# Kernel tuning notes

Measured on AMD Instinct MI355X. Metric: run time of the kernel, lower is better.

## Reference

```python
import jax, jax.numpy as jnp
import numpy as np

IB = 8      # input/hidden activation bits
ABMVM = 8   # gate activation bits after MVM
ABNM = 8    # near-memory compute bits
NL = 0.05   # analog noise level
CY_DIV = 2.0
CY_SCALE = 2.0


def quant_pass(x, wb, sign):
    # Faithful port of QuantFunc.forward: clip/clamp then fake-quant (round to grid).
    if wb is None or wb == 0:
        return x
    if sign:
        delta = 0.0 if wb == 1 else 1.0 / (2.0 ** (wb - 1))
        x = jnp.clip(x, -1.0 + delta, 1.0 - delta)
    else:
        x = jnp.clip(x, 0.0, 1.0)
    if wb == 1:
        return jnp.sign(x)
    scale = 2.0 ** (wb - 1) if sign else 2.0 ** wb
    return jnp.round(x * scale) / scale


def setup_inputs() -> dict:
    key = jax.random.key(0)
    ks = jax.random.split(key, 7)
    B, I, H = 4096, 1024, 1024
    return {
        "input": jax.random.normal(ks[0], (B, I), jnp.float32),
        "hx": jax.random.normal(ks[1], (B, H), jnp.float32),
        "cx": jax.random.normal(ks[2], (B, H), jnp.float32),
        "weight_ih": jax.random.normal(ks[3], (4 * H, I), jnp.float32) * 0.1,
        "weight_hh": jax.random.normal(ks[4], (4 * H, H), jnp.float32) * 0.1,
        "bias_ih": jax.random.normal(ks[5], (4 * H,), jnp.float32) * 0.1,
        "bias_hh": jax.random.normal(ks[6], (4 * H,), jnp.float32) * 0.1,
        "train": 0,
    }


def reference(input, hx, cx, weight_ih, weight_hh, bias_ih, bias_hh, train):
    # Per-call Gaussian noise (simulated analog hardware); fixed key for reproducibility.
    nk = jax.random.split(jax.random.key(42), 4)
    noise_w_ih = jax.random.normal(nk[0], weight_ih.T.shape, weight_ih.dtype) * weight_ih.max() * NL
    noise_w_hh = jax.random.normal(nk[1], weight_hh.T.shape, weight_hh.dtype) * weight_hh.max() * NL
    noise_b_ih = jax.random.normal(nk[2], bias_ih.shape, bias_ih.dtype) * bias_ih.max() * NL
    noise_b_hh = jax.random.normal(nk[3], bias_hh.shape, bias_hh.dtype) * bias_hh.max() * NL

    # gates: [B, 4H]
    gates = (quant_pass(input, IB, True) @ (weight_ih.T + noise_w_ih) + bias_ih + noise_b_ih
             + quant_pass(hx, IB, True) @ (weight_hh.T + noise_w_hh) + bias_hh + noise_b_hh)

    ingate, forgetgate, cellgate, outgate = jnp.split(gates, 4, axis=1)
    ingate = quant_pass(jax.nn.sigmoid(ingate), ABMVM, False)
    forgetgate = quant_pass(jax.nn.sigmoid(forgetgate), ABMVM, False)
    cellgate = quant_pass(jnp.tanh(cellgate), ABMVM, True)
    outgate = quant_pass(jax.nn.sigmoid(outgate), ABMVM, False)

    cy = quant_pass((quant_pass(forgetgate * cx, ABNM, True)
                     + quant_pass(ingate * cellgate, ABNM, True)) / CY_DIV, ABNM, True)
    hy = quant_pass(outgate * quant_pass(jnp.tanh(cy * CY_SCALE), ABNM, True), ABNM, True)
    return (hy, cy)
```

## Files before the change

### kernel.cpp

```cpp
#include <hip/hip_runtime.h>
#include <hip/hip_bf16.h>
#include <stdint.h>
#include <stddef.h>


#define PART 1

typedef __attribute__((ext_vector_type(8))) short bf16x8;
typedef __attribute__((ext_vector_type(4))) float f32x4;

#define BATCH 4096

#define WS_A_OFF    ((size_t)0)
#define WS_B_OFF    ((size_t)16 << 20)
#define WS_BIAS_OFF ((size_t)48 << 20)
#define WS_MAX_OFF  (WS_BIAS_OFF + 16384)

__host__ __device__ inline void tf2x32(uint32_t k0, uint32_t k1,
                                       uint32_t x0, uint32_t x1,
                                       uint32_t &o0, uint32_t &o1)
{
  const uint32_t k2 = k0 ^ k1 ^ 0x1BD11BDAu;
#define TFR(r) { x0 += x1; x1 = (x1 << (r)) | (x1 >> (32 - (r))); x1 ^= x0; }
  x0 += k0; x1 += k1;
  TFR(13) TFR(15) TFR(26) TFR(6)
  x0 += k1; x1 += k2 + 1u;
  TFR(17) TFR(29) TFR(16) TFR(24)
  x0 += k2; x1 += k0 + 2u;
  TFR(13) TFR(15) TFR(26) TFR(6)
  x0 += k0; x1 += k1 + 3u;
  TFR(17) TFR(29) TFR(16) TFR(24)
  x0 += k1; x1 += k2 + 4u;
  TFR(13) TFR(15) TFR(26) TFR(6)
  x0 += k2; x1 += k0 + 5u;
#undef TFR
  o0 = x0; o1 = x1;
}

__device__ inline uint32_t jax_bits32(uint32_t k0, uint32_t k1, uint32_t i, uint32_t size)
{
#if PART
  uint32_t a, b;
  tf2x32(k0, k1, 0u, i, a, b);
  return a ^ b;
#else
  uint32_t half = size >> 1, a, b;
  if (i < half) { tf2x32(k0, k1, i, i + half, a, b); return a; }
  tf2x32(k0, k1, i - half, i, a, b); return b;
#endif
}

__device__ inline float bits_to_normal(uint32_t bits)
{
  float f = __uint_as_float((bits >> 9) | 0x3F800000u) - 1.0f;
  const float lo = -0x1.fffffep-1f;
  float u = fmaxf(lo, f * 2.0f + lo);
  float w = -log1pf(-u * u);
  float p;
  if (w < 5.0f) {
    w -= 2.5f;
    p = 2.81022636e-08f;
    p = fmaf(p, w, 3.43273939e-07f);
    p = fmaf(p, w, -3.5233877e-06f);
    p = fmaf(p, w, -4.39150654e-06f);
    p = fmaf(p, w, 0.00021858087f);
    p = fmaf(p, w, -0.00125372503f);
    p = fmaf(p, w, -0.00417768164f);
    p = fmaf(p, w, 0.246640727f);
    p = fmaf(p, w, 1.50140941f);
  } else {
    w = sqrtf(w) - 3.0f;
    p = -0.000200214257f;
    p = fmaf(p, w, 0.000100950558f);
    p = fmaf(p, w, 0.00134934322f);
    p = fmaf(p, w, -0.00367342844f);
    p = fmaf(p, w, 0.00573950773f);
    p = fmaf(p, w, -0.0076224613f);
    p = fmaf(p, w, 0.00943887047f);
    p = fmaf(p, w, 1.00167406f);
    p = fmaf(p, w, 2.83297682f);
  }
  return 0x1.6a09e6p+0f * (p * u);
}

__device__ inline float quantS8(float x)
{
  x = fminf(fmaxf(x, -0.9921875f), 0.9921875f);
  return rintf(x * 128.0f) * 0.0078125f;
}
__device__ inline float quantU8(float x)
{
  x = fminf(fmaxf(x, 0.0f), 1.0f);
  return rintf(x * 256.0f) * 0.00390625f;
}

#define LOG2E 1.44269504088896340736f
__device__ inline float sigmoid_fast(float x)
{
  float e = __builtin_amdgcn_exp2f(x * -LOG2E);
  return __builtin_amdgcn_rcpf(1.0f + e);
}
__device__ inline float tanh_fast(float x)
{
  float a = fabsf(x);
  float e = __builtin_amdgcn_exp2f(a * (-2.0f * LOG2E));
  float t = (1.0f - e) * __builtin_amdgcn_rcpf(1.0f + e);
  return copysignf(t, x);
}

__device__ inline unsigned short f2bf(float x)
{
  uint32_t b = __float_as_uint(x);
  return (unsigned short)((b + 0x7FFFu + ((b >> 16) & 1u)) >> 16);
}
__device__ inline float bf2f(unsigned short u) { return __uint_as_float(((uint32_t)u) << 16); }

__device__ inline float dec_max(uint32_t u)
{
  uint32_t bits = (u & 0x80000000u) ? (u ^ 0x80000000u) : ~u;
  return __uint_as_float(bits);
}

__global__ void init_max(uint32_t* mx)
{
  if (threadIdx.x < 4) mx[threadIdx.x] = 0u;
}

__global__ void kmax_all(const float4* __restrict__ wih, const float4* __restrict__ whh,
                         const float4* __restrict__ bih, const float4* __restrict__ bhh,
                         uint32_t* __restrict__ mx)
{
  const int blk = blockIdx.x;
  const float4* src; int n4, bl, nb; uint32_t* out;
  if (blk < 1024)      { src = wih; n4 = 1048576; bl = blk;        nb = 1024; out = mx + 0; }
  else if (blk < 2048) { src = whh; n4 = 1048576; bl = blk - 1024; nb = 1024; out = mx + 1; }
  else if (blk < 2052) { src = bih; n4 = 1024;    bl = blk - 2048; nb = 4;    out = mx + 2; }
  else                 { src = bhh; n4 = 1024;    bl = blk - 2052; nb = 4;    out = mx + 3; }

  float m = -3.4e38f;
  for (int i = bl * 256 + threadIdx.x; i < n4; i += nb * 256) {
    float4 v = src[i];
    m = fmaxf(fmaxf(m, fmaxf(v.x, v.y)), fmaxf(v.z, v.w));
  }
  for (int off = 32; off; off >>= 1) m = fmaxf(m, __shfl_down(m, off, 64));
  __shared__ float sm[4];
  if ((threadIdx.x & 63) == 0) sm[threadIdx.x >> 6] = m;
  __syncthreads();
  if (threadIdx.x == 0) {
    float bm = fmaxf(fmaxf(sm[0], sm[1]), fmaxf(sm[2], sm[3]));
    uint32_t bits = __float_as_uint(bm);
    uint32_t enc = (bits & 0x80000000u) ? ~bits : (bits | 0x80000000u);
    atomicMax(out, enc);
  }
}

__global__ void build_all(const float* __restrict__ wih, const float* __restrict__ whh,
                          const float4* __restrict__ in, const float4* __restrict__ hxp,
                          const float* __restrict__ bih, const float* __restrict__ bhh,
                          unsigned short* __restrict__ A, unsigned short* __restrict__ B,
                          float* __restrict__ biasE, const uint32_t* __restrict__ mxenc,
                          uint32_t kih0, uint32_t kih1, uint32_t khh0, uint32_t khh1,
                          uint32_t kbi0, uint32_t kbi1, uint32_t kbh0, uint32_t kbh1)
{
  const uint32_t blk = blockIdx.x;
  if (blk < 32768u) {
    uint32_t t = blk * 256u + threadIdx.x;
    uint32_t arr = t >> 22;
    uint32_t r = t & 4194303u;
    uint32_t k = r & 1023u;
    uint32_t n = r >> 10;
    const float* w = arr ? whh : wih;
    float mx = dec_max(mxenc[arr]);
    uint32_t key0 = arr ? khh0 : kih0, key1 = arr ? khh1 : kih1;
    uint32_t i = k * 4096u + n;
    float nrm = bits_to_normal(jax_bits32(key0, key1, i, 4194304u));
    float weff = w[(size_t)n * 1024u + k] + (nrm * mx) * 0.05f;
    unsigned short hi = f2bf(weff);
    unsigned short lob = f2bf(weff - bf2f(hi));
    uint32_t np = (n & 1023u) * 4u + (n >> 10);
    size_t base = (size_t)np * 4096u + (arr ? 1024u : 0u) + k;
    B[base] = hi;
    B[base + 2048u] = lob;
  } else if (blk < 40960u) {
    int t = (int)(blk - 32768u) * 256 + threadIdx.x;
    int b = t >> 9;
    int kq = t & 511;
    float4 v = (kq < 256) ? in[b * 256 + kq] : hxp[b * 256 + (kq - 256)];
    unsigned short o[4];
    o[0] = f2bf(quantS8(v.x)); o[1] = f2bf(quantS8(v.y));
    o[2] = f2bf(quantS8(v.z)); o[3] = f2bf(quantS8(v.w));
    *reinterpret_cast<uint64_t*>(A + (size_t)t * 4) = *reinterpret_cast<uint64_t*>(o);
  } else {
    uint32_t j = (blk - 40960u) * 256u + threadIdx.x;
    float mi = dec_max(mxenc[2]), mh = dec_max(mxenc[3]);
    float ni = (bits_to_normal(jax_bits32(kbi0, kbi1, j, 4096u)) * mi) * 0.05f;
    float nh = (bits_to_normal(jax_bits32(kbh0, kbh1, j, 4096u)) * mh) * 0.05f;
    biasE[(j & 1023u) * 4u + (j >> 10)] = ((bih[j] + ni) + bhh[j]) + nh;
  }
}

__device__ __forceinline__ void gload_lds16(const void* g, void* l)
{
  __builtin_amdgcn_global_load_lds((__attribute__((address_space(1))) void*)g,
                                   (__attribute__((address_space(3))) void*)l, 16, 0, 0);
}

#define VM6  asm volatile("s_waitcnt vmcnt(6)" ::: "memory")
#define VM0  asm volatile("s_waitcnt vmcnt(0)" ::: "memory")
#define NOVM
#define SBAR __builtin_amdgcn_s_barrier()
#define SCB  __builtin_amdgcn_sched_barrier(0)

#define BUFSZ 49152

#define STAGE_A(ts_, bi_)                                                         \
    { unsigned char* la_ = lds + (bi_) * BUFSZ; const int ka_ = (ts_) * 32;       \
      gload_lds16(Ar0 + ka_, la_ + tid * 16);                                     \
      gload_lds16(Ar1 + ka_, la_ + 8192 + tid * 16); }
#define STAGE_BH(ts_, bi_)                                                        \
    { unsigned char* la_ = lds + (bi_) * BUFSZ; const int ka_ = (ts_) * 32;       \
      gload_lds16(Br0 + ka_, la_ + 16384 + tid * 16);                             \
      gload_lds16(Br1 + ka_, la_ + 16384 + 8192 + tid * 16); }
#define STAGE_BL(ts_, bi_)                                                        \
    { unsigned char* la_ = lds + (bi_) * BUFSZ; const int ka_ = (ts_) * 32;       \
      gload_lds16(Br0 + 2048 + ka_, la_ + 32768 + tid * 16);                      \
      gload_lds16(Br1 + 2048 + ka_, la_ + 32768 + 8192 + tid * 16); }

#define TILE_ONE(t_, BUF_, BUFN_, DO_STAGE_, VM_ASM_)                             \
  {                                                                               \
    const unsigned char* pa_  = lds + (BUF_) * BUFSZ + aoff;                      \
    const unsigned char* pbh_ = lds + (BUF_) * BUFSZ + 16384 + boffU;             \
    const unsigned char* pbl_ = lds + (BUF_) * BUFSZ + 32768 + boffU;             \
    bf16x8 bh_[4], bl_[4], afL_[4], afH_[4];                                      \
    _Pragma("unroll") for (int n_ = 0; n_ < 4; ++n_)                              \
      bh_[n_] = *(const bf16x8*)(pbh_ + n_ * 1024);                               \
    _Pragma("unroll") for (int m_ = 0; m_ < 4; ++m_)                              \
      afL_[m_] = *(const bf16x8*)(pa_ + m_ * 1024);                               \
    if (DO_STAGE_) STAGE_A((t_) + 2, BUFN_);                                      \
    SBAR; SCB;                                                                    \
    __builtin_amdgcn_s_setprio(1);                                                \
    _Pragma("unroll") for (int m_ = 0; m_ < 4; ++m_)                              \
      _Pragma("unroll") for (int n_ = 0; n_ < 4; ++n_)                            \
        acc[m_][n_] = __builtin_amdgcn_mfma_f32_16x16x32_bf16(afL_[m_], bh_[n_],  \
                                                              acc[m_][n_], 0, 0, 0); \
    __builtin_amdgcn_s_setprio(0);                                                \
    SBAR; SCB;                                                                    \
    _Pragma("unroll") for (int m_ = 0; m_ < 4; ++m_)                              \
      afH_[m_] = *(const bf16x8*)(pa_ + (4 + m_) * 1024);                         \
    if (DO_STAGE_) STAGE_BH((t_) + 2, BUFN_);                                     \
    SBAR; SCB;                                                                    \
    __builtin_amdgcn_s_setprio(1);                                                \
    _Pragma("unroll") for (int m_ = 0; m_ < 4; ++m_)                              \
      _Pragma("unroll") for (int n_ = 0; n_ < 4; ++n_)                            \
        acc[4 + m_][n_] = __builtin_amdgcn_mfma_f32_16x16x32_bf16(afH_[m_], bh_[n_], \
                                                              acc[4 + m_][n_], 0, 0, 0); \
    __builtin_amdgcn_s_setprio(0);                                                \
    SBAR; SCB;                                                                    \
    _Pragma("unroll") for (int n_ = 0; n_ < 4; ++n_)                              \
      bl_[n_] = *(const bf16x8*)(pbl_ + n_ * 1024);                               \
    if (DO_STAGE_) STAGE_BL((t_) + 2, BUFN_);                                     \
    SBAR; SCB;                                                                    \
    __builtin_amdgcn_s_setprio(1);                                                \
    _Pragma("unroll") for (int m_ = 0; m_ < 4; ++m_)                              \
      _Pragma("unroll") for (int n_ = 0; n_ < 4; ++n_)                            \
        acc[m_][n_] = __builtin_amdgcn_mfma_f32_16x16x32_bf16(afL_[m_], bl_[n_],  \
                                                              acc[m_][n_], 0, 0, 0); \
    _Pragma("unroll") for (int m_ = 0; m_ < 4; ++m_)                              \
      _Pragma("unroll") for (int n_ = 0; n_ < 4; ++n_)                            \
        acc[4 + m_][n_] = __builtin_amdgcn_mfma_f32_16x16x32_bf16(afH_[m_], bl_[n_], \
                                                              acc[4 + m_][n_], 0, 0, 0); \
    __builtin_amdgcn_s_setprio(0);                                                \
    VM_ASM_;                                                                      \
    SBAR; SCB;                                                                    \
  }

#define LTS 272

__global__ __launch_bounds__(512, 2) void gemm_gates(
    const unsigned short* __restrict__ A,
    const unsigned short* __restrict__ B,
    const float* __restrict__ bias,
    const float* __restrict__ cx,
    float* __restrict__ hy,
    float* __restrict__ cy)
{
  extern __shared__ unsigned char lds[];
  const int tid  = threadIdx.x;
  const int lane = tid & 63;
  const int wave = tid >> 6;
  const int wr = wave >> 2;
  const int wc = wave & 3;

  const int bid = blockIdx.x;
  const int wg  = (bid & 7) * 32 + (bid >> 3);
  const int brow = (wg & 15) * 256;
  const int bcol = (wg >> 4) * 256;

  int sr0, sk0, sr1, sk1;
  {
    int c = tid, p = c >> 3, lc = (c & 7) ^ (p & 7);
    sr0 = p * 2 + (lc >> 2); sk0 = (lc & 3) * 8;
    c = tid + 512; p = c >> 3; lc = (c & 7) ^ (p & 7);
    sr1 = p * 2 + (lc >> 2); sk1 = (lc & 3) * 8;
  }
  const unsigned short* Ar0 = A + (size_t)(brow + sr0) * 2048 + sk0;
  const unsigned short* Ar1 = A + (size_t)(brow + sr1) * 2048 + sk1;
  const unsigned short* Br0 = B + (size_t)(bcol + sr0) * 4096 + sk0;
  const unsigned short* Br1 = B + (size_t)(bcol + sr1) * 4096 + sk1;

  const int lrh = (lane & 15) >> 1;
  const int chk = ((((lane & 1) << 2) | (lane >> 4)) ^ lrh);
  const int aoff  = wr * 8192 + lrh * 128 + chk * 16;
  const int boffU = wc * 4096 + lrh * 128 + chk * 16;

  f32x4 acc[8][4] = {};

  STAGE_A(0, 0); STAGE_BH(0, 0); STAGE_BL(0, 0);
  STAGE_A(1, 1); STAGE_BH(1, 1); STAGE_BL(1, 1);
  VM6;
  SBAR; SCB;

#pragma unroll 1
  for (int tt = 0; tt < 60; tt += 3) {
    TILE_ONE(tt + 0, 0, 2, 1, VM6);
    TILE_ONE(tt + 1, 1, 0, 1, VM6);
    TILE_ONE(tt + 2, 2, 1, 1, VM6);
  }
  TILE_ONE(60, 0, 2, 1, VM6);
  TILE_ONE(61, 1, 0, 1, VM6);
  TILE_ONE(62, 2, 0, 0, VM0);
  TILE_ONE(63, 0, 0, 0, NOVM);

  float* LT = (float*)lds;
  const int col_local0 = wc * 64 + (lane & 15);
  const int lrow = (lane >> 4) << 2;
  const int h = tid & 63;
  const int hg = (bcol >> 2) + h;

#pragma unroll
  for (int hh = 0; hh < 2; ++hh) {
    __syncthreads();
#pragma unroll
    for (int m = 0; m < 4; ++m) {
#pragma unroll
      for (int n = 0; n < 4; ++n) {
        const int cl = col_local0 + n * 16;
        const float bv = bias[bcol + cl];
        const int lr0 = wr * 64 + m * 16 + lrow;
#pragma unroll
        for (int r = 0; r < 4; ++r)
          LT[(lr0 + r) * LTS + cl] = acc[hh * 4 + m][n][r] + bv;
      }
    }
    __syncthreads();
#pragma unroll
    for (int i = 0; i < 16; ++i) {
      const int lr = (tid >> 6) * 16 + i;
      const int grow = brow + ((lr >> 6) << 7) + hh * 64 + (lr & 63);
      const float4 q = *(const float4*)(LT + lr * LTS + 4 * h);
      const size_t oidx = (size_t)grow * 1024 + hg;
      float ing = quantU8(sigmoid_fast(q.x));
      float fg  = quantU8(sigmoid_fast(q.y));
      float cg  = quantS8(tanh_fast(q.z));
      float og  = quantU8(sigmoid_fast(q.w));
      float c0  = cx[oidx];
      float cyv = quantS8((quantS8(fg * c0) + quantS8(ing * cg)) * 0.5f);
      float hyv = quantS8(og * quantS8(tanh_fast(cyv * 2.0f)));
      hy[oidx] = hyv;
      cy[oidx] = cyv;
    }
  }
}

extern "C" void kernel_launch(void* const* d_in, const int* in_sizes, int n_in,
                              void* d_out, int out_size, void* d_ws, size_t ws_size,
                              hipStream_t stream)
{
  const float* input = (const float*)d_in[0];
  const float* hx    = (const float*)d_in[1];
  const float* cx    = (const float*)d_in[2];
  const float* wih   = (const float*)d_in[3];
  const float* whh   = (const float*)d_in[4];
  const float* bih   = (const float*)d_in[5];
  const float* bhh   = (const float*)d_in[6];
  (void)in_sizes; (void)n_in; (void)ws_size;

  uint8_t* ws = (uint8_t*)d_ws;
  unsigned short* A   = (unsigned short*)(ws + WS_A_OFF);
  unsigned short* B   = (unsigned short*)(ws + WS_B_OFF);
  float* biasE        = (float*)(ws + WS_BIAS_OFF);
  uint32_t* mx        = (uint32_t*)(ws + WS_MAX_OFF);

  uint32_t nk[4][2];
#if PART
  for (int i = 0; i < 4; ++i) tf2x32(0u, 42u, 0u, (uint32_t)i, nk[i][0], nk[i][1]);
#else
  {
    uint32_t w0[4], w1[4];
    for (int i = 0; i < 4; ++i) tf2x32(0u, 42u, (uint32_t)i, (uint32_t)(i + 4), w0[i], w1[i]);
    uint32_t out8[8] = {w0[0], w0[1], w0[2], w0[3], w1[0], w1[1], w1[2], w1[3]};
    for (int i = 0; i < 4; ++i) { nk[i][0] = out8[2 * i]; nk[i][1] = out8[2 * i + 1]; }
  }
#endif

  init_max<<<1, 64, 0, stream>>>(mx);
  kmax_all<<<2056, 256, 0, stream>>>((const float4*)wih, (const float4*)whh,
                                     (const float4*)bih, (const float4*)bhh, mx);
  build_all<<<40976, 256, 0, stream>>>(wih, whh, (const float4*)input, (const float4*)hx,
                                       bih, bhh, A, B, biasE, mx,
                                       nk[0][0], nk[0][1], nk[1][0], nk[1][1],
                                       nk[2][0], nk[2][1], nk[3][0], nk[3][1]);

  float* hy = (float*)d_out;
  float* cyp = hy + (size_t)BATCH * 1024;

  (void)hipFuncSetAttribute((const void*)gemm_gates,
                            hipFuncAttributeMaxDynamicSharedMemorySize, 147456);
  gemm_gates<<<dim3(256), dim3(512), 147456, stream>>>(A, B, biasE, cx, hy, cyp);
}
```

Baseline: 190.5 us.

## Shrink GEMM tile to 256x128 with 4 waves and double-buffered LDS pipeline

Halves the output tile width per block (256x128), cuts threads from 512 to 256 (4 waves), and launches 512 blocks instead of 256. The LDS pipeline goes from triple buffering with prefetch distance two to double buffering with prefetch distance one, and it waits on vmcnt(0) every tile. The aim is more blocks per CU and better load balance across the 256 CUs. In exchange, the smaller tile gives each block less reuse of the B operand, and the fully drained loads every tile expose more memory latency.

```diff
diff --git a/kernel.cpp b/kernel.cpp
--- a/kernel.cpp
+++ b/kernel.cpp
@@ -205,38 +205,39 @@
                                    (__attribute__((address_space(3))) void*)l, 16, 0, 0);
 }
 
-#define VM6  asm volatile("s_waitcnt vmcnt(6)" ::: "memory")
 #define VM0  asm volatile("s_waitcnt vmcnt(0)" ::: "memory")
 #define NOVM
 #define SBAR __builtin_amdgcn_s_barrier()
 #define SCB  __builtin_amdgcn_sched_barrier(0)
 
-#define BUFSZ 49152
+#define BUFSZ 32768
 
 #define STAGE_A(ts_, bi_)                                                         \
     { unsigned char* la_ = lds + (bi_) * BUFSZ; const int ka_ = (ts_) * 32;       \
       gload_lds16(Ar0 + ka_, la_ + tid * 16);                                     \
-      gload_lds16(Ar1 + ka_, la_ + 8192 + tid * 16); }
+      gload_lds16(Ar1 + ka_, la_ + 4096 + tid * 16);                              \
+      gload_lds16(Ar2 + ka_, la_ + 8192 + tid * 16);                              \
+      gload_lds16(Ar3 + ka_, la_ + 12288 + tid * 16); }
 #define STAGE_BH(ts_, bi_)                                                        \
     { unsigned char* la_ = lds + (bi_) * BUFSZ; const int ka_ = (ts_) * 32;       \
       gload_lds16(Br0 + ka_, la_ + 16384 + tid * 16);                             \
-      gload_lds16(Br1 + ka_, la_ + 16384 + 8192 + tid * 16); }
+      gload_lds16(Br1 + ka_, la_ + 16384 + 4096 + tid * 16); }
 #define STAGE_BL(ts_, bi_)                                                        \
     { unsigned char* la_ = lds + (bi_) * BUFSZ; const int ka_ = (ts_) * 32;       \
-      gload_lds16(Br0 + 2048 + ka_, la_ + 32768 + tid * 16);                      \
-      gload_lds16(Br1 + 2048 + ka_, la_ + 32768 + 8192 + tid * 16); }
+      gload_lds16(Br0 + 2048 + ka_, la_ + 24576 + tid * 16);                      \
+      gload_lds16(Br1 + 2048 + ka_, la_ + 24576 + 4096 + tid * 16); }
 
 #define TILE_ONE(t_, BUF_, BUFN_, DO_STAGE_, VM_ASM_)                             \
   {                                                                               \
     const unsigned char* pa_  = lds + (BUF_) * BUFSZ + aoff;                      \
     const unsigned char* pbh_ = lds + (BUF_) * BUFSZ + 16384 + boffU;             \
-    const unsigned char* pbl_ = lds + (BUF_) * BUFSZ + 32768 + boffU;             \
+    const unsigned char* pbl_ = lds + (BUF_) * BUFSZ + 24576 + boffU;             \
     bf16x8 bh_[4], bl_[4], afL_[4], afH_[4];                                      \
     _Pragma("unroll") for (int n_ = 0; n_ < 4; ++n_)                              \
       bh_[n_] = *(const bf16x8*)(pbh_ + n_ * 1024);                               \
     _Pragma("unroll") for (int m_ = 0; m_ < 4; ++m_)                              \
       afL_[m_] = *(const bf16x8*)(pa_ + m_ * 1024);                               \
-    if (DO_STAGE_) STAGE_A((t_) + 2, BUFN_);                                      \
+    if (DO_STAGE_) STAGE_A((t_) + 1, BUFN_);                                      \
     SBAR; SCB;                                                                    \
     __builtin_amdgcn_s_setprio(1);                                                \
     _Pragma("unroll") for (int m_ = 0; m_ < 4; ++m_)                              \
@@ -247,7 +248,7 @@
     SBAR; SCB;                                                                    \
     _Pragma("unroll") for (int m_ = 0; m_ < 4; ++m_)                              \
       afH_[m_] = *(const bf16x8*)(pa_ + (4 + m_) * 1024);                         \
-    if (DO_STAGE_) STAGE_BH((t_) + 2, BUFN_);                                     \
+    if (DO_STAGE_) STAGE_BH((t_) + 1, BUFN_);                                     \
     SBAR; SCB;                                                                    \
     __builtin_amdgcn_s_setprio(1);                                                \
     _Pragma("unroll") for (int m_ = 0; m_ < 4; ++m_)                              \
@@ -258,7 +259,7 @@
     SBAR; SCB;                                                                    \
     _Pragma("unroll") for (int n_ = 0; n_ < 4; ++n_)                              \
       bl_[n_] = *(const bf16x8*)(pbl_ + n_ * 1024);                               \
-    if (DO_STAGE_) STAGE_BL((t_) + 2, BUFN_);                                     \
+    if (DO_STAGE_) STAGE_BL((t_) + 1, BUFN_);                                     \
     SBAR; SCB;                                                                    \
     __builtin_amdgcn_s_setprio(1);                                                \
     _Pragma("unroll") for (int m_ = 0; m_ < 4; ++m_)                              \
@@ -274,9 +275,9 @@
     SBAR; SCB;                                                                    \
   }
 
-#define LTS 272
-
-__global__ __launch_bounds__(512, 2) void gemm_gates(
+#define LTS 136
+
+__global__ __launch_bounds__(256, 2) void gemm_gates(
     const unsigned short* __restrict__ A,
     const unsigned short* __restrict__ B,
     const float* __restrict__ bias,
@@ -288,25 +289,29 @@
   const int tid  = threadIdx.x;
   const int lane = tid & 63;
   const int wave = tid >> 6;
-  const int wr = wave >> 2;
-  const int wc = wave & 3;
+  const int wr = wave >> 1;
+  const int wc = wave & 1;
 
   const int bid = blockIdx.x;
-  const int wg  = (bid & 7) * 32 + (bid >> 3);
+  const int wg  = (bid & 7) * 64 + (bid >> 3);
   const int brow = (wg & 15) * 256;
-  const int bcol = (wg >> 4) * 256;
-
-  int sr0, sk0, sr1, sk1;
-  {
-    int c = tid, p = c >> 3, lc = (c & 7) ^ (p & 7);
-    sr0 = p * 2 + (lc >> 2); sk0 = (lc & 3) * 8;
-    c = tid + 512; p = c >> 3; lc = (c & 7) ^ (p & 7);
-    sr1 = p * 2 + (lc >> 2); sk1 = (lc & 3) * 8;
-  }
-  const unsigned short* Ar0 = A + (size_t)(brow + sr0) * 2048 + sk0;
-  const unsigned short* Ar1 = A + (size_t)(brow + sr1) * 2048 + sk1;
-  const unsigned short* Br0 = B + (size_t)(bcol + sr0) * 4096 + sk0;
-  const unsigned short* Br1 = B + (size_t)(bcol + sr1) * 4096 + sk1;
+  const int bcol = (wg >> 4) * 128;
+
+#define CHUNK_SRC(c_, sr_, sk_) \
+    { int p_ = (c_) >> 3, lc_ = ((c_) & 7) ^ (p_ & 7); \
+      sr_ = p_ * 2 + (lc_ >> 2); sk_ = (lc_ & 3) * 8; }
+  int sr, sk;
+  CHUNK_SRC(tid,        sr, sk);
+  const unsigned short* Ar0 = A + (size_t)(brow + sr) * 2048 + sk;
+  const unsigned short* Br0 = B + (size_t)(bcol + sr) * 4096 + sk;
+  CHUNK_SRC(tid + 256,  sr, sk);
+  const unsigned short* Ar1 = A + (size_t)(brow + sr) * 2048 + sk;
+  const unsigned short* Br1 = B + (size_t)(bcol + sr) * 4096 + sk;
+  CHUNK_SRC(tid + 512,  sr, sk);
+  const unsigned short* Ar2 = A + (size_t)(brow + sr) * 2048 + sk;
+  CHUNK_SRC(tid + 768,  sr, sk);
+  const unsigned short* Ar3 = A + (size_t)(brow + sr) * 2048 + sk;
+#undef CHUNK_SRC
 
   const int lrh = (lane & 15) >> 1;
   const int chk = ((((lane & 1) << 2) | (lane >> 4)) ^ lrh);
@@ -316,25 +321,19 @@
   f32x4 acc[8][4] = {};
 
   STAGE_A(0, 0); STAGE_BH(0, 0); STAGE_BL(0, 0);
-  STAGE_A(1, 1); STAGE_BH(1, 1); STAGE_BL(1, 1);
-  VM6;
+  VM0;
   SBAR; SCB;
 
 #pragma unroll 1
-  for (int tt = 0; tt < 60; tt += 3) {
-    TILE_ONE(tt + 0, 0, 2, 1, VM6);
-    TILE_ONE(tt + 1, 1, 0, 1, VM6);
-    TILE_ONE(tt + 2, 2, 1, 1, VM6);
-  }
-  TILE_ONE(60, 0, 2, 1, VM6);
-  TILE_ONE(61, 1, 0, 1, VM6);
-  TILE_ONE(62, 2, 0, 0, VM0);
-  TILE_ONE(63, 0, 0, 0, NOVM);
+  for (int t = 0; t < 63; ++t) {
+    TILE_ONE(t, (t & 1), ((t + 1) & 1), 1, VM0);
+  }
+  TILE_ONE(63, 1, 0, 0, NOVM);
 
   float* LT = (float*)lds;
   const int col_local0 = wc * 64 + (lane & 15);
   const int lrow = (lane >> 4) << 2;
-  const int h = tid & 63;
+  const int h = tid & 31;
   const int hg = (bcol >> 2) + h;
 
 #pragma unroll
@@ -355,7 +354,7 @@
     __syncthreads();
 #pragma unroll
     for (int i = 0; i < 16; ++i) {
-      const int lr = (tid >> 6) * 16 + i;
+      const int lr = (tid >> 5) * 16 + i;
       const int grow = brow + ((lr >> 6) << 7) + hh * 64 + (lr & 63);
       const float4 q = *(const float4*)(LT + lr * LTS + 4 * h);
       const size_t oidx = (size_t)grow * 1024 + hg;
@@ -415,6 +414,6 @@
   float* cyp = hy + (size_t)BATCH * 1024;
 
   (void)hipFuncSetAttribute((const void*)gemm_gates,
-                            hipFuncAttributeMaxDynamicSharedMemorySize, 147456);
-  gemm_gates<<<dim3(256), dim3(512), 147456, stream>>>(A, B, biasE, cx, hy, cyp);
-}
+                            hipFuncAttributeMaxDynamicSharedMemorySize, 71680);
+  gemm_gates<<<dim3(512), dim3(256), 71680, stream>>>(A, B, biasE, cx, hy, cyp);
+}
```

Result: no change. 193.7 us (+1.7%).
